# Performance work log

Hardware: AMD Instinct MI355X
Metric: run time of the kernel (lower is better)

The kernel has to match this reference:

```python
import jax, jax.numpy as jnp
import numpy as np

H = 256
T = 2048
B = 64


def setup_inputs() -> dict:
    key = jax.random.key(0)
    ks = jax.random.split(key, 10)
    s = 1.0 / np.sqrt(H)
    return {
        "x": jax.random.normal(ks[0], (T, B, H), dtype=jnp.float32),
        # AttentionLayer params
        "W_b": jax.random.normal(ks[1], (H, H), dtype=jnp.float32) * s,
        "b_b": jnp.zeros((H,), dtype=jnp.float32),
        "v_b": jax.random.normal(ks[2], (1, H), dtype=jnp.float32) * s,
        "W_e": jax.random.normal(ks[3], (H, 2 * H), dtype=jnp.float32) * s,
        "b_e": jnp.zeros((H,), dtype=jnp.float32),
        # LSTMCell params (PyTorch layout: [4H, H], gate order i,f,g,o)
        "W_ih": jax.random.uniform(ks[4], (4 * H, H), dtype=jnp.float32, minval=-s, maxval=s),
        "W_hh": jax.random.uniform(ks[5], (4 * H, H), dtype=jnp.float32, minval=-s, maxval=s),
        "b_ih": jax.random.uniform(ks[6], (4 * H,), dtype=jnp.float32, minval=-s, maxval=s),
        "b_hh": jax.random.uniform(ks[7], (4 * H,), dtype=jnp.float32, minval=-s, maxval=s),
    }


def reference(x, W_b, b_b, v_b, W_e, b_e, W_ih, W_hh, b_ih, b_hh):
    # x: [T, B, H]. Effective recurrence per timestep (inner per-sample loop in
    # the original is dead code: its output writes are overwritten and its
    # states start from zeros each iteration).
    def step(carry, xi):
        h, c = carry  # [B, H] each
        hc = jnp.concatenate([h, c], axis=1)  # [B, 2H]
        a = hc @ W_e.T + b_e                  # [B, H]
        b = xi @ W_b.T + b_b                  # [B, H]
        j = jnp.tanh(a + b) @ v_b.T           # [B, 1]
        w = jax.nn.softmax(j, axis=0) * xi    # softmax over batch dim, [B, H]
        gates = w @ W_ih.T + b_ih + h @ W_hh.T + b_hh  # [B, 4H]
        i_g, f_g, g_g, o_g = jnp.split(gates, 4, axis=1)
        c_new = jax.nn.sigmoid(f_g) * c + jax.nn.sigmoid(i_g) * jnp.tanh(g_g)
        h_new = jax.nn.sigmoid(o_g) * jnp.tanh(c_new)
        return (h_new, c_new), h_new

    Bn, Hn = x.shape[1], x.shape[2]
    init = (jnp.zeros((Bn, Hn), x.dtype), jnp.zeros((Bn, Hn), x.dtype))
    _, output = jax.lax.scan(step, init, x)  # [T, B, H]
    return output
```

## Files before the change

### kernel.cpp

```cpp
#include <hip/hip_runtime.h>
#include <math.h>

constexpr int H   = 256;
constexpr int B   = 64;
constexpr int T   = 2048;
constexpr int G   = 64;
constexpr int NTH = 512;
constexpr int HB  = H * B;

struct SharedMain {
    float wU[256][16];
    float wV[256][16];
    float wA[768][4];
    float U[64][17];
    float V[64][17];
    float ap[64][5];
    alignas(16) float outst[64][4];
    float jp[8][64];
    float bg[16];
    float ba[4];
    float v4[4];
    float s[64];
};
union SharedAll {
    SharedMain m;
    float tile[64][65];
};

__device__ __forceinline__ float sigmoidf_(float v) {
    return 1.0f / (1.0f + expf(-v));
}

__device__ __forceinline__ void grid_barrier(unsigned* bar, unsigned target) {
    __syncthreads();
    if (threadIdx.x == 0) {
        __threadfence();
        __hip_atomic_fetch_add(bar, 1u, __ATOMIC_ACQ_REL, __HIP_MEMORY_SCOPE_AGENT);
        while (__hip_atomic_load(bar, __ATOMIC_ACQUIRE, __HIP_MEMORY_SCOPE_AGENT) < target) {
            __builtin_amdgcn_s_sleep(1);
        }
        __threadfence();
    }
    __syncthreads();
}

__global__ void __launch_bounds__(NTH, 1)
scan_kernel(const float* __restrict__ x,
            const float* __restrict__ W_b,  const float* __restrict__ b_b,
            const float* __restrict__ v_b,  const float* __restrict__ W_e,
            const float* __restrict__ b_e,  const float* __restrict__ W_ih,
            const float* __restrict__ W_hh, const float* __restrict__ b_ih,
            const float* __restrict__ b_hh,
            float* __restrict__ out, float* __restrict__ wsf,
            unsigned* __restrict__ bar)
{
    __shared__ SharedAll sh;
    const int tid = threadIdx.x;
    const int g   = blockIdx.x;

    float* pJ = wsf + 64;
    float* hT = pJ + G * 64;
    float* cT = hT + HB;
    float* xT = out;

    for (int tl = g; tl < T * 4; tl += G) {
        const int t  = tl >> 2;
        const int kc = (tl & 3) << 6;
        __syncthreads();
        for (int q = tid; q < 1024; q += NTH) {
            const int r  = q >> 4;
            const int c4 = (q & 15) << 2;
            const float4 v = *(const float4*)(x + (size_t)t * HB + (size_t)r * H + kc + c4);
            sh.tile[r][c4 + 0] = v.x; sh.tile[r][c4 + 1] = v.y;
            sh.tile[r][c4 + 2] = v.z; sh.tile[r][c4 + 3] = v.w;
        }
        __syncthreads();
        for (int q = tid; q < 1024; q += NTH) {
            const int k  = q >> 4;
            const int b4 = (q & 15) << 2;
            float4 v;
            v.x = sh.tile[b4 + 0][k]; v.y = sh.tile[b4 + 1][k];
            v.z = sh.tile[b4 + 2][k]; v.w = sh.tile[b4 + 3][k];
            *(float4*)(xT + (size_t)t * HB + (size_t)(kc + k) * B + b4) = v;
        }
    }
    __syncthreads();

    for (int e = tid; e < 256 * 16; e += NTH) {
        const int k  = e >> 4;
        const int cl = e & 15;
        const int gate = cl >> 2, oi = cl & 3;
        const int row = gate * H + 4 * g + oi;
        sh.m.wU[k][cl] = W_ih[(size_t)row * H + k];
        sh.m.wV[k][cl] = W_hh[(size_t)row * H + k];
    }
    for (int e = tid; e < 768 * 4; e += NTH) {
        const int r = e >> 2;
        const int i = e & 3;
        const int col = 4 * g + i;
        float w;
        if (r < 512) w = W_e[(size_t)col * 512 + r];
        else         w = W_b[(size_t)col * 256 + (r - 512)];
        sh.m.wA[r][i] = w;
    }
    if (tid < 16) {
        const int gate = tid >> 2, oi = tid & 3;
        const int col = gate * H + 4 * g + oi;
        sh.m.bg[tid] = b_ih[col] + b_hh[col];
    }
    if (tid < 4) {
        sh.m.ba[tid] = b_e[4 * g + tid] + b_b[4 * g + tid];
        sh.m.v4[tid] = v_b[4 * g + tid];
    }
    hT[g * NTH + tid] = 0.0f;

    unsigned nb = 0;
    ++nb; grid_barrier(bar, nb * (unsigned)G);

    const int wv = tid >> 6;
    const int b  = tid & 63;

    for (int t = 0; t < T; ++t) {
        for (int e = tid; e < 64 * 17; e += NTH) { (&sh.m.U[0][0])[e] = 0.0f; (&sh.m.V[0][0])[e] = 0.0f; }
        for (int e = tid; e < 64 * 5; e += NTH) (&sh.m.ap[0][0])[e] = 0.0f;
        __syncthreads();

        if (wv < 4) {
            const int krow = wv << 6;
            const float* src = xT + (size_t)t * HB + (size_t)krow * B;
            float aU[16], aA[4];
            #pragma unroll
            for (int c = 0; c < 16; ++c) aU[c] = 0.0f;
            aA[0] = aA[1] = aA[2] = aA[3] = 0.0f;
            #pragma unroll 4
            for (int kk = 0; kk < 64; ++kk) {
                const float xv = src[kk * B + b];
                const float* wr = sh.m.wU[krow + kk];
                #pragma unroll
                for (int c = 0; c < 16; ++c) aU[c] = fmaf(xv, wr[c], aU[c]);
                const float* wa = sh.m.wA[512 + krow + kk];
                #pragma unroll
                for (int i = 0; i < 4; ++i) aA[i] = fmaf(xv, wa[i], aA[i]);
            }
            #pragma unroll
            for (int c = 0; c < 16; ++c) atomicAdd(&sh.m.U[b][c], aU[c]);
            #pragma unroll
            for (int i = 0; i < 4; ++i) atomicAdd(&sh.m.ap[b][i], aA[i]);
        } else {
            const int krow = (wv - 4) << 6;
            const float* sH = hT + (size_t)krow * B;
            const float* sC = cT + (size_t)krow * B;
            float aV[16], aA[4];
            #pragma unroll
            for (int c = 0; c < 16; ++c) aV[c] = 0.0f;
            aA[0] = aA[1] = aA[2] = aA[3] = 0.0f;
            #pragma unroll 4
            for (int kk = 0; kk < 64; ++kk) {
                const float hv = sH[kk * B + b];
                const float cv = sC[kk * B + b];
                const float* wr = sh.m.wV[krow + kk];
                #pragma unroll
                for (int c = 0; c < 16; ++c) aV[c] = fmaf(hv, wr[c], aV[c]);
                const float* waH = sh.m.wA[krow + kk];
                const float* waC = sh.m.wA[256 + krow + kk];
                #pragma unroll
                for (int i = 0; i < 4; ++i) aA[i] = fmaf(hv, waH[i], fmaf(cv, waC[i], aA[i]));
            }
            #pragma unroll
            for (int c = 0; c < 16; ++c) atomicAdd(&sh.m.V[b][c], aV[c]);
            #pragma unroll
            for (int i = 0; i < 4; ++i) atomicAdd(&sh.m.ap[b][i], aA[i]);
        }
        __syncthreads();

        if (tid < 64) {
            float pj = 0.0f;
            #pragma unroll
            for (int i = 0; i < 4; ++i)
                pj += tanhf(sh.m.ap[tid][i] + sh.m.ba[i]) * sh.m.v4[i];
            pJ[g * 64 + tid] = pj;
        }
        ++nb; grid_barrier(bar, nb * (unsigned)G);

        {
            float jpart = 0.0f;
            const int base = wv * 8;
            #pragma unroll
            for (int gg = 0; gg < 8; ++gg) jpart += pJ[(base + gg) * 64 + b];
            sh.m.jp[wv][b] = jpart;
        }
        __syncthreads();
        if (tid < 64) {
            float jv = 0.0f;
            #pragma unroll
            for (int w = 0; w < 8; ++w) jv += sh.m.jp[w][tid];
            float mx = jv;
            #pragma unroll
            for (int off = 32; off; off >>= 1) mx = fmaxf(mx, __shfl_xor(mx, off));
            const float e = expf(jv - mx);
            float ssum = e;
            #pragma unroll
            for (int off = 32; off; off >>= 1) ssum += __shfl_xor(ssum, off);
            sh.m.s[tid] = e / ssum;
        }
        __syncthreads();

        if (tid < 256) {
            const int oi = tid >> 6;
            const int bb = tid & 63;
            const float sb = sh.m.s[bb];
            const float pI = fmaf(sb, sh.m.U[bb][0  + oi], sh.m.V[bb][0  + oi]) + sh.m.bg[0  + oi];
            const float pF = fmaf(sb, sh.m.U[bb][4  + oi], sh.m.V[bb][4  + oi]) + sh.m.bg[4  + oi];
            const float pG = fmaf(sb, sh.m.U[bb][8  + oi], sh.m.V[bb][8  + oi]) + sh.m.bg[8  + oi];
            const float pO = fmaf(sb, sh.m.U[bb][12 + oi], sh.m.V[bb][12 + oi]) + sh.m.bg[12 + oi];
            const int col = 4 * g + oi;
            const float cold = cT[col * B + bb];
            const float cnew = sigmoidf_(pF) * cold + sigmoidf_(pI) * tanhf(pG);
            const float hnew = sigmoidf_(pO) * tanhf(cnew);
            cT[col * B + bb] = cnew;
            hT[col * B + bb] = hnew;
            sh.m.outst[bb][oi] = hnew;
        }
        __syncthreads();
        if (tid < 64) {
            const float4 v = *(const float4*)sh.m.outst[tid];
            *(float4*)(out + (size_t)t * HB + (size_t)tid * H + 4 * g) = v;
        }
        ++nb; grid_barrier(bar, nb * (unsigned)G);
    }
}

extern "C" void kernel_launch(void* const* d_in, const int* in_sizes, int n_in,
                              void* d_out, int out_size, void* d_ws, size_t ws_size,
                              hipStream_t stream) {
    const float* x    = (const float*)d_in[0];
    const float* W_b  = (const float*)d_in[1];
    const float* b_b  = (const float*)d_in[2];
    const float* v_b  = (const float*)d_in[3];
    const float* W_e  = (const float*)d_in[4];
    const float* b_e  = (const float*)d_in[5];
    const float* W_ih = (const float*)d_in[6];
    const float* W_hh = (const float*)d_in[7];
    const float* b_ih = (const float*)d_in[8];
    const float* b_hh = (const float*)d_in[9];
    float*    out = (float*)d_out;
    float*    wsf = (float*)d_ws;
    unsigned* bar = (unsigned*)d_ws;

    hipMemsetAsync(d_ws, 0, 256, stream);

    void* args[] = { &x, &W_b, &b_b, &v_b, &W_e, &b_e, &W_ih, &W_hh, &b_ih, &b_hh,
                     &out, &wsf, &bar };
    hipLaunchCooperativeKernel((void*)scan_kernel, dim3(G), dim3(NTH), args, 0, stream);
}
```

Baseline: 89.88 ms.

## Overlap next-step x projection with grid barrier waits using split arrive/wait epochs

Replaces the full grid barriers with split arrive/wait epoch counters, so each block signals arrival and then computes the x-dependent projection for the next timestep (double-buffered in shared memory) while other blocks catch up. All 8 waves now share the h/c recurrent reduction instead of half doing x and half doing h. The cell state is kept in shared memory rather than re-read from global. Global h/c/pJ traffic uses relaxed agent-scope atomic loads and stores with no fences, which risks memory-ordering issues. The added shared buffers raise LDS use.

```diff
diff --git a/kernel.cpp b/kernel.cpp
--- a/kernel.cpp
+++ b/kernel.cpp
@@ -12,11 +12,13 @@
     float wU[256][16];
     float wV[256][16];
     float wA[768][4];
-    float U[64][17];
+    float U[2][64][17];
+    float aX[2][64][5];
     float V[64][17];
-    float ap[64][5];
+    float aH[64][5];
     alignas(16) float outst[64][4];
     float jp[8][64];
+    float cloc[4][64];
     float bg[16];
     float ba[4];
     float v4[4];
@@ -31,7 +33,14 @@
     return 1.0f / (1.0f + expf(-v));
 }
 
-__device__ __forceinline__ void grid_barrier(unsigned* bar, unsigned target) {
+__device__ __forceinline__ float gload(const float* p) {
+    return __hip_atomic_load(p, __ATOMIC_RELAXED, __HIP_MEMORY_SCOPE_AGENT);
+}
+__device__ __forceinline__ void gstore(float* p, float v) {
+    __hip_atomic_store(p, v, __ATOMIC_RELAXED, __HIP_MEMORY_SCOPE_AGENT);
+}
+
+__device__ __forceinline__ void grid_barrier_full(unsigned* bar, unsigned target) {
     __syncthreads();
     if (threadIdx.x == 0) {
         __threadfence();
@@ -42,6 +51,18 @@
         __threadfence();
     }
     __syncthreads();
+}
+
+__device__ __forceinline__ void epoch_wait(unsigned* bar, unsigned target) {
+    if (threadIdx.x == 0) {
+        while (__hip_atomic_load(bar, __ATOMIC_RELAXED, __HIP_MEMORY_SCOPE_AGENT) < target) {
+            __builtin_amdgcn_s_sleep(1);
+        }
+    }
+    __syncthreads();
+}
+__device__ __forceinline__ void epoch_arrive(unsigned* bar) {
+    __hip_atomic_fetch_add(bar, 1u, __ATOMIC_RELAXED, __HIP_MEMORY_SCOPE_AGENT);
 }
 
 __global__ void __launch_bounds__(NTH, 1)
@@ -57,6 +78,8 @@
     __shared__ SharedAll sh;
     const int tid = threadIdx.x;
     const int g   = blockIdx.x;
+    const int wv  = tid >> 6;
+    const int b   = tid & 63;
 
     float* pJ = wsf + 64;
     float* hT = pJ + G * 64;
@@ -114,50 +137,59 @@
     }
     hT[g * NTH + tid] = 0.0f;
 
-    unsigned nb = 0;
-    ++nb; grid_barrier(bar, nb * (unsigned)G);
-
-    const int wv = tid >> 6;
-    const int b  = tid & 63;
+    grid_barrier_full(bar, (unsigned)G);
+
+    auto x_zero = [&](int p) {
+        for (int e = tid; e < 64 * 17; e += NTH) (&sh.m.U[p][0][0])[e] = 0.0f;
+        for (int e = tid; e < 64 * 5;  e += NTH) (&sh.m.aX[p][0][0])[e] = 0.0f;
+    };
+    auto x_accum = [&](int t, int p, int half) {
+        const int krow = (wv << 4) + (half << 7);
+        const float* src = xT + (size_t)t * HB + (size_t)krow * B;
+        float aU[16], aA[4];
+        #pragma unroll
+        for (int c = 0; c < 16; ++c) aU[c] = 0.0f;
+        aA[0] = aA[1] = aA[2] = aA[3] = 0.0f;
+        #pragma unroll 4
+        for (int kk = 0; kk < 16; ++kk) {
+            const float xv = src[kk * B + b];
+            const float* wr = sh.m.wU[krow + kk];
+            #pragma unroll
+            for (int c = 0; c < 16; ++c) aU[c] = fmaf(xv, wr[c], aU[c]);
+            const float* wa = sh.m.wA[512 + krow + kk];
+            #pragma unroll
+            for (int i = 0; i < 4; ++i) aA[i] = fmaf(xv, wa[i], aA[i]);
+        }
+        #pragma unroll
+        for (int c = 0; c < 16; ++c) atomicAdd(&sh.m.U[p][b][c], aU[c]);
+        #pragma unroll
+        for (int i = 0; i < 4; ++i) atomicAdd(&sh.m.aX[p][b][i], aA[i]);
+    };
+
+    int par = 0;
+    if (tid < 256) sh.m.cloc[tid >> 6][tid & 63] = 0.0f;
+    for (int e = tid; e < 64 * 17; e += NTH) (&sh.m.V[0][0])[e] = 0.0f;
+    for (int e = tid; e < 64 * 5;  e += NTH) (&sh.m.aH[0][0])[e] = 0.0f;
+    x_zero(0);
+    __syncthreads();
+    x_accum(0, 0, 0);
+    x_accum(0, 0, 1);
 
     for (int t = 0; t < T; ++t) {
-        for (int e = tid; e < 64 * 17; e += NTH) { (&sh.m.U[0][0])[e] = 0.0f; (&sh.m.V[0][0])[e] = 0.0f; }
-        for (int e = tid; e < 64 * 5; e += NTH) (&sh.m.ap[0][0])[e] = 0.0f;
-        __syncthreads();
-
-        if (wv < 4) {
-            const int krow = wv << 6;
-            const float* src = xT + (size_t)t * HB + (size_t)krow * B;
-            float aU[16], aA[4];
-            #pragma unroll
-            for (int c = 0; c < 16; ++c) aU[c] = 0.0f;
-            aA[0] = aA[1] = aA[2] = aA[3] = 0.0f;
-            #pragma unroll 4
-            for (int kk = 0; kk < 64; ++kk) {
-                const float xv = src[kk * B + b];
-                const float* wr = sh.m.wU[krow + kk];
-                #pragma unroll
-                for (int c = 0; c < 16; ++c) aU[c] = fmaf(xv, wr[c], aU[c]);
-                const float* wa = sh.m.wA[512 + krow + kk];
-                #pragma unroll
-                for (int i = 0; i < 4; ++i) aA[i] = fmaf(xv, wa[i], aA[i]);
-            }
-            #pragma unroll
-            for (int c = 0; c < 16; ++c) atomicAdd(&sh.m.U[b][c], aU[c]);
-            #pragma unroll
-            for (int i = 0; i < 4; ++i) atomicAdd(&sh.m.ap[b][i], aA[i]);
-        } else {
-            const int krow = (wv - 4) << 6;
-            const float* sH = hT + (size_t)krow * B;
-            const float* sC = cT + (size_t)krow * B;
+        if (t > 0) epoch_wait(bar, (unsigned)(2 * t + 1) * G);
+
+        {
+            const int krow = wv << 5;
+            const float* sHp = hT + (size_t)krow * B;
+            const float* sCp = cT + (size_t)krow * B;
             float aV[16], aA[4];
             #pragma unroll
             for (int c = 0; c < 16; ++c) aV[c] = 0.0f;
             aA[0] = aA[1] = aA[2] = aA[3] = 0.0f;
-            #pragma unroll 4
-            for (int kk = 0; kk < 64; ++kk) {
-                const float hv = sH[kk * B + b];
-                const float cv = sC[kk * B + b];
+            #pragma unroll 8
+            for (int kk = 0; kk < 32; ++kk) {
+                const float hv = gload(sHp + kk * B + b);
+                const float cv = gload(sCp + kk * B + b);
                 const float* wr = sh.m.wV[krow + kk];
                 #pragma unroll
                 for (int c = 0; c < 16; ++c) aV[c] = fmaf(hv, wr[c], aV[c]);
@@ -169,7 +201,7 @@
             #pragma unroll
             for (int c = 0; c < 16; ++c) atomicAdd(&sh.m.V[b][c], aV[c]);
             #pragma unroll
-            for (int i = 0; i < 4; ++i) atomicAdd(&sh.m.ap[b][i], aA[i]);
+            for (int i = 0; i < 4; ++i) atomicAdd(&sh.m.aH[b][i], aA[i]);
         }
         __syncthreads();
 
@@ -177,16 +209,21 @@
             float pj = 0.0f;
             #pragma unroll
             for (int i = 0; i < 4; ++i)
-                pj += tanhf(sh.m.ap[tid][i] + sh.m.ba[i]) * sh.m.v4[i];
-            pJ[g * 64 + tid] = pj;
-        }
-        ++nb; grid_barrier(bar, nb * (unsigned)G);
+                pj += tanhf(sh.m.aX[par][tid][i] + sh.m.aH[tid][i] + sh.m.ba[i]) * sh.m.v4[i];
+            gstore(&pJ[g * 64 + tid], pj);
+        }
+        __syncthreads();
+        if (tid == 0) epoch_arrive(bar);
+
+        if (t + 1 < T) { x_zero(par ^ 1); __syncthreads(); x_accum(t + 1, par ^ 1, 0); }
+
+        epoch_wait(bar, (unsigned)(2 * t + 2) * G);
 
         {
             float jpart = 0.0f;
             const int base = wv * 8;
             #pragma unroll
-            for (int gg = 0; gg < 8; ++gg) jpart += pJ[(base + gg) * 64 + b];
+            for (int gg = 0; gg < 8; ++gg) jpart += gload(&pJ[(base + gg) * 64 + b]);
             sh.m.jp[wv][b] = jpart;
         }
         __syncthreads();
@@ -209,24 +246,34 @@
             const int oi = tid >> 6;
             const int bb = tid & 63;
             const float sb = sh.m.s[bb];
-            const float pI = fmaf(sb, sh.m.U[bb][0  + oi], sh.m.V[bb][0  + oi]) + sh.m.bg[0  + oi];
-            const float pF = fmaf(sb, sh.m.U[bb][4  + oi], sh.m.V[bb][4  + oi]) + sh.m.bg[4  + oi];
-            const float pG = fmaf(sb, sh.m.U[bb][8  + oi], sh.m.V[bb][8  + oi]) + sh.m.bg[8  + oi];
-            const float pO = fmaf(sb, sh.m.U[bb][12 + oi], sh.m.V[bb][12 + oi]) + sh.m.bg[12 + oi];
+            const float* Ur = sh.m.U[par][bb];
+            const float* Vr = sh.m.V[bb];
+            const float pI = fmaf(sb, Ur[0  + oi], Vr[0  + oi]) + sh.m.bg[0  + oi];
+            const float pF = fmaf(sb, Ur[4  + oi], Vr[4  + oi]) + sh.m.bg[4  + oi];
+            const float pG = fmaf(sb, Ur[8  + oi], Vr[8  + oi]) + sh.m.bg[8  + oi];
+            const float pO = fmaf(sb, Ur[12 + oi], Vr[12 + oi]) + sh.m.bg[12 + oi];
             const int col = 4 * g + oi;
-            const float cold = cT[col * B + bb];
+            const float cold = sh.m.cloc[oi][bb];
             const float cnew = sigmoidf_(pF) * cold + sigmoidf_(pI) * tanhf(pG);
             const float hnew = sigmoidf_(pO) * tanhf(cnew);
-            cT[col * B + bb] = cnew;
-            hT[col * B + bb] = hnew;
+            sh.m.cloc[oi][bb] = cnew;
+            gstore(&cT[(size_t)col * B + bb], cnew);
+            gstore(&hT[(size_t)col * B + bb], hnew);
             sh.m.outst[bb][oi] = hnew;
         }
         __syncthreads();
+
         if (tid < 64) {
             const float4 v = *(const float4*)sh.m.outst[tid];
             *(float4*)(out + (size_t)t * HB + (size_t)tid * H + 4 * g) = v;
         }
-        ++nb; grid_barrier(bar, nb * (unsigned)G);
+        for (int e = tid; e < 64 * 17; e += NTH) (&sh.m.V[0][0])[e] = 0.0f;
+        for (int e = tid; e < 64 * 5;  e += NTH) (&sh.m.aH[0][0])[e] = 0.0f;
+        __syncthreads();
+        if (tid == 0) epoch_arrive(bar);
+
+        if (t + 1 < T) x_accum(t + 1, par ^ 1, 1);
+        par ^= 1;
     }
 }
 
```

After: 118.9 ms. 1.32x slower.

## Partition recurrence by batch sample per block with flag-based softmax exchange

Applied to the files above, without the earlier changes.

Each block now owns one batch sample and keeps its full h and c in shared memory. The old split across hidden columns needed two grid barriers per step and global h/c traffic; the only cross-block exchange left is the per-sample attention score, published through versioned 64-bit slots that a single wave polls. Weights are streamed from global memory/L2 every step instead of being held in LDS, and the next step's x·W_b projection is computed ahead of time. The x transpose prologue is also removed.

```diff
diff --git a/kernel.cpp b/kernel.cpp
--- a/kernel.cpp
+++ b/kernel.cpp
@@ -5,43 +5,32 @@
 constexpr int B   = 64;
 constexpr int T   = 2048;
 constexpr int G   = 64;
-constexpr int NTH = 512;
+constexpr int NTH = 1024;
 constexpr int HB  = H * B;
 
-struct SharedMain {
-    float wU[256][16];
-    float wV[256][16];
-    float wA[768][4];
-    float U[64][17];
-    float V[64][17];
-    float ap[64][5];
-    alignas(16) float outst[64][4];
-    float jp[8][64];
-    float bg[16];
-    float ba[4];
-    float v4[4];
-    float s[64];
+struct Sh {
+    float h[H];
+    float c[H];
+    float xv[2][H];
+    float bx[2][H];
+    float a_s[H];
+    float Ux[4*H];
+    float Vh[4*H];
+    float bg[4*H];
+    float ba[H];
+    float vb[H];
+    float jp[4];
+    float sb;
 };
-union SharedAll {
-    SharedMain m;
-    float tile[64][65];
-};
-
-__device__ __forceinline__ float sigmoidf_(float v) {
-    return 1.0f / (1.0f + expf(-v));
-}
-
-__device__ __forceinline__ void grid_barrier(unsigned* bar, unsigned target) {
-    __syncthreads();
-    if (threadIdx.x == 0) {
-        __threadfence();
-        __hip_atomic_fetch_add(bar, 1u, __ATOMIC_ACQ_REL, __HIP_MEMORY_SCOPE_AGENT);
-        while (__hip_atomic_load(bar, __ATOMIC_ACQUIRE, __HIP_MEMORY_SCOPE_AGENT) < target) {
-            __builtin_amdgcn_s_sleep(1);
-        }
-        __threadfence();
-    }
-    __syncthreads();
+
+__device__ __forceinline__ float sigmoidf_(float v) { return 1.0f / (1.0f + expf(-v)); }
+
+__device__ __forceinline__ float dot4(float4 w, float4 m, float acc) {
+    acc = fmaf(w.x, m.x, acc);
+    acc = fmaf(w.y, m.y, acc);
+    acc = fmaf(w.z, m.z, acc);
+    acc = fmaf(w.w, m.w, acc);
+    return acc;
 }
 
 __global__ void __launch_bounds__(NTH, 1)
@@ -51,182 +40,159 @@
             const float* __restrict__ b_e,  const float* __restrict__ W_ih,
             const float* __restrict__ W_hh, const float* __restrict__ b_ih,
             const float* __restrict__ b_hh,
-            float* __restrict__ out, float* __restrict__ wsf,
-            unsigned* __restrict__ bar)
+            float* __restrict__ out,
+            unsigned long long* __restrict__ slot)
 {
-    __shared__ SharedAll sh;
-    const int tid = threadIdx.x;
-    const int g   = blockIdx.x;
-
-    float* pJ = wsf + 64;
-    float* hT = pJ + G * 64;
-    float* cT = hT + HB;
-    float* xT = out;
-
-    for (int tl = g; tl < T * 4; tl += G) {
-        const int t  = tl >> 2;
-        const int kc = (tl & 3) << 6;
-        __syncthreads();
-        for (int q = tid; q < 1024; q += NTH) {
-            const int r  = q >> 4;
-            const int c4 = (q & 15) << 2;
-            const float4 v = *(const float4*)(x + (size_t)t * HB + (size_t)r * H + kc + c4);
-            sh.tile[r][c4 + 0] = v.x; sh.tile[r][c4 + 1] = v.y;
-            sh.tile[r][c4 + 2] = v.z; sh.tile[r][c4 + 3] = v.w;
-        }
-        __syncthreads();
-        for (int q = tid; q < 1024; q += NTH) {
-            const int k  = q >> 4;
-            const int b4 = (q & 15) << 2;
-            float4 v;
-            v.x = sh.tile[b4 + 0][k]; v.y = sh.tile[b4 + 1][k];
-            v.z = sh.tile[b4 + 2][k]; v.w = sh.tile[b4 + 3][k];
-            *(float4*)(xT + (size_t)t * HB + (size_t)(kc + k) * B + b4) = v;
-        }
+    __shared__ Sh sh;
+    const int tid  = threadIdx.x;
+    const int g    = blockIdx.x;
+    const int wv   = tid >> 6;
+    const int lane = tid & 63;
+    const int oct  = lane >> 3;
+    const int q    = lane & 7;
+
+    sh.bg[tid] = b_ih[tid] + b_hh[tid];
+    if (tid < H) {
+        sh.h[tid] = 0.0f; sh.c[tid] = 0.0f;
+        sh.ba[tid] = b_e[tid] + b_b[tid];
+        sh.vb[tid] = v_b[tid];
+    }
+    if (tid < 64) {
+        float4 v = *(const float4*)(x + (size_t)g * H + (size_t)tid * 4);
+        *(float4*)&sh.xv[0][tid * 4] = v;
     }
     __syncthreads();
-
-    for (int e = tid; e < 256 * 16; e += NTH) {
-        const int k  = e >> 4;
-        const int cl = e & 15;
-        const int gate = cl >> 2, oi = cl & 3;
-        const int row = gate * H + 4 * g + oi;
-        sh.m.wU[k][cl] = W_ih[(size_t)row * H + k];
-        sh.m.wV[k][cl] = W_hh[(size_t)row * H + k];
-    }
-    for (int e = tid; e < 768 * 4; e += NTH) {
-        const int r = e >> 2;
-        const int i = e & 3;
-        const int col = 4 * g + i;
-        float w;
-        if (r < 512) w = W_e[(size_t)col * 512 + r];
-        else         w = W_b[(size_t)col * 256 + (r - 512)];
-        sh.m.wA[r][i] = w;
-    }
-    if (tid < 16) {
-        const int gate = tid >> 2, oi = tid & 3;
-        const int col = gate * H + 4 * g + oi;
-        sh.m.bg[tid] = b_ih[col] + b_hh[col];
-    }
-    if (tid < 4) {
-        sh.m.ba[tid] = b_e[4 * g + tid] + b_b[4 * g + tid];
-        sh.m.v4[tid] = v_b[4 * g + tid];
-    }
-    hT[g * NTH + tid] = 0.0f;
-
-    unsigned nb = 0;
-    ++nb; grid_barrier(bar, nb * (unsigned)G);
-
-    const int wv = tid >> 6;
-    const int b  = tid & 63;
-
+    {
+        const float4* xv4 = (const float4*)sh.xv[0];
+        #pragma unroll
+        for (int p = 0; p < 2; ++p) {
+            const int r = wv * 16 + p * 8 + oct;
+            const float4* wr4 = (const float4*)(W_b + (size_t)r * H);
+            float acc = 0.0f;
+            #pragma unroll
+            for (int j = 0; j < 8; ++j)
+                acc = dot4(wr4[j * 8 + q], xv4[j * 8 + q], acc);
+            acc += __shfl_xor(acc, 1); acc += __shfl_xor(acc, 2); acc += __shfl_xor(acc, 4);
+            if (q == 0) sh.bx[0][r] = acc;
+        }
+    }
+    __syncthreads();
+
+    int par = 0;
     for (int t = 0; t < T; ++t) {
-        for (int e = tid; e < 64 * 17; e += NTH) { (&sh.m.U[0][0])[e] = 0.0f; (&sh.m.V[0][0])[e] = 0.0f; }
-        for (int e = tid; e < 64 * 5; e += NTH) (&sh.m.ap[0][0])[e] = 0.0f;
-        __syncthreads();
-
-        if (wv < 4) {
-            const int krow = wv << 6;
-            const float* src = xT + (size_t)t * HB + (size_t)krow * B;
-            float aU[16], aA[4];
-            #pragma unroll
-            for (int c = 0; c < 16; ++c) aU[c] = 0.0f;
-            aA[0] = aA[1] = aA[2] = aA[3] = 0.0f;
-            #pragma unroll 4
-            for (int kk = 0; kk < 64; ++kk) {
-                const float xv = src[kk * B + b];
-                const float* wr = sh.m.wU[krow + kk];
-                #pragma unroll
-                for (int c = 0; c < 16; ++c) aU[c] = fmaf(xv, wr[c], aU[c]);
-                const float* wa = sh.m.wA[512 + krow + kk];
-                #pragma unroll
-                for (int i = 0; i < 4; ++i) aA[i] = fmaf(xv, wa[i], aA[i]);
-            }
-            #pragma unroll
-            for (int c = 0; c < 16; ++c) atomicAdd(&sh.m.U[b][c], aU[c]);
-            #pragma unroll
-            for (int i = 0; i < 4; ++i) atomicAdd(&sh.m.ap[b][i], aA[i]);
-        } else {
-            const int krow = (wv - 4) << 6;
-            const float* sH = hT + (size_t)krow * B;
-            const float* sC = cT + (size_t)krow * B;
-            float aV[16], aA[4];
-            #pragma unroll
-            for (int c = 0; c < 16; ++c) aV[c] = 0.0f;
-            aA[0] = aA[1] = aA[2] = aA[3] = 0.0f;
-            #pragma unroll 4
-            for (int kk = 0; kk < 64; ++kk) {
-                const float hv = sH[kk * B + b];
-                const float cv = sC[kk * B + b];
-                const float* wr = sh.m.wV[krow + kk];
-                #pragma unroll
-                for (int c = 0; c < 16; ++c) aV[c] = fmaf(hv, wr[c], aV[c]);
-                const float* waH = sh.m.wA[krow + kk];
-                const float* waC = sh.m.wA[256 + krow + kk];
-                #pragma unroll
-                for (int i = 0; i < 4; ++i) aA[i] = fmaf(hv, waH[i], fmaf(cv, waC[i], aA[i]));
-            }
-            #pragma unroll
-            for (int c = 0; c < 16; ++c) atomicAdd(&sh.m.V[b][c], aV[c]);
-            #pragma unroll
-            for (int i = 0; i < 4; ++i) atomicAdd(&sh.m.ap[b][i], aA[i]);
-        }
-        __syncthreads();
-
+        {
+            const float4* hv4 = (const float4*)sh.h;
+            const float4* cv4 = (const float4*)sh.c;
+            #pragma unroll
+            for (int p = 0; p < 2; ++p) {
+                const int r = wv * 16 + p * 8 + oct;
+                const float4* wr4 = (const float4*)(W_e + (size_t)r * (2 * H));
+                float acc = 0.0f;
+                #pragma unroll
+                for (int j = 0; j < 8; ++j)
+                    acc = dot4(wr4[j * 8 + q], hv4[j * 8 + q], acc);
+                #pragma unroll
+                for (int j = 0; j < 8; ++j)
+                    acc = dot4(wr4[64 + j * 8 + q], cv4[j * 8 + q], acc);
+                acc += __shfl_xor(acc, 1); acc += __shfl_xor(acc, 2); acc += __shfl_xor(acc, 4);
+                if (q == 0) sh.a_s[r] = acc;
+            }
+        }
+        __syncthreads();
+        if (tid < H) {
+            float tv = tanhf(sh.a_s[tid] + sh.bx[par][tid] + sh.ba[tid]) * sh.vb[tid];
+            #pragma unroll
+            for (int off = 32; off; off >>= 1) tv += __shfl_xor(tv, off);
+            if (lane == 0) sh.jp[wv] = tv;
+        }
+        __syncthreads();
+        if (tid == 0) {
+            float jv = sh.jp[0] + sh.jp[1] + sh.jp[2] + sh.jp[3];
+            unsigned long long u = ((unsigned long long)(unsigned)(t + 1) << 32)
+                                 | (unsigned long long)__float_as_uint(jv);
+            __hip_atomic_store(&slot[(size_t)(t & 1) * G + g], u,
+                               __ATOMIC_RELAXED, __HIP_MEMORY_SCOPE_AGENT);
+        }
+
+        const int parn = par ^ 1;
+        const int tn = (t + 1 < T) ? (t + 1) : t;
         if (tid < 64) {
-            float pj = 0.0f;
-            #pragma unroll
-            for (int i = 0; i < 4; ++i)
-                pj += tanhf(sh.m.ap[tid][i] + sh.m.ba[i]) * sh.m.v4[i];
-            pJ[g * 64 + tid] = pj;
-        }
-        ++nb; grid_barrier(bar, nb * (unsigned)G);
-
+            float4 v = *(const float4*)(x + ((size_t)tn * B + g) * H + (size_t)tid * 4);
+            *(float4*)&sh.xv[parn][tid * 4] = v;
+        }
         {
-            float jpart = 0.0f;
-            const int base = wv * 8;
-            #pragma unroll
-            for (int gg = 0; gg < 8; ++gg) jpart += pJ[(base + gg) * 64 + b];
-            sh.m.jp[wv][b] = jpart;
-        }
-        __syncthreads();
-        if (tid < 64) {
-            float jv = 0.0f;
-            #pragma unroll
-            for (int w = 0; w < 8; ++w) jv += sh.m.jp[w][tid];
+            const float4* xv4 = (const float4*)sh.xv[par];
+            const float4* hv4 = (const float4*)sh.h;
+            #pragma unroll 2
+            for (int p = 0; p < 8; ++p) {
+                const int r = wv * 64 + p * 8 + oct;
+                const float4* wi4 = (const float4*)(W_ih + (size_t)r * H);
+                const float4* wh4 = (const float4*)(W_hh + (size_t)r * H);
+                float aU = 0.0f, aV = 0.0f;
+                #pragma unroll
+                for (int j = 0; j < 8; ++j) {
+                    const float4 xm = xv4[j * 8 + q];
+                    const float4 hm = hv4[j * 8 + q];
+                    aU = dot4(wi4[j * 8 + q], xm, aU);
+                    aV = dot4(wh4[j * 8 + q], hm, aV);
+                }
+                aU += __shfl_xor(aU, 1); aU += __shfl_xor(aU, 2); aU += __shfl_xor(aU, 4);
+                aV += __shfl_xor(aV, 1); aV += __shfl_xor(aV, 2); aV += __shfl_xor(aV, 4);
+                if (q == 0) { sh.Ux[r] = aU; sh.Vh[r] = aV; }
+            }
+        }
+        __syncthreads();
+        {
+            const float4* xv4 = (const float4*)sh.xv[parn];
+            #pragma unroll
+            for (int p = 0; p < 2; ++p) {
+                const int r = wv * 16 + p * 8 + oct;
+                const float4* wr4 = (const float4*)(W_b + (size_t)r * H);
+                float acc = 0.0f;
+                #pragma unroll
+                for (int j = 0; j < 8; ++j)
+                    acc = dot4(wr4[j * 8 + q], xv4[j * 8 + q], acc);
+                acc += __shfl_xor(acc, 1); acc += __shfl_xor(acc, 2); acc += __shfl_xor(acc, 4);
+                if (q == 0) sh.bx[parn][r] = acc;
+            }
+        }
+
+        if (wv == 0) {
+            const unsigned want = (unsigned)(t + 1);
+            unsigned long long u;
+            for (;;) {
+                u = __hip_atomic_load(&slot[(size_t)(t & 1) * G + lane],
+                                      __ATOMIC_RELAXED, __HIP_MEMORY_SCOPE_AGENT);
+                if (__all((int)((unsigned)(u >> 32) == want))) break;
+                __builtin_amdgcn_s_sleep(1);
+            }
+            float jv = __uint_as_float((unsigned)u);
             float mx = jv;
             #pragma unroll
             for (int off = 32; off; off >>= 1) mx = fmaxf(mx, __shfl_xor(mx, off));
-            const float e = expf(jv - mx);
-            float ssum = e;
-            #pragma unroll
-            for (int off = 32; off; off >>= 1) ssum += __shfl_xor(ssum, off);
-            sh.m.s[tid] = e / ssum;
-        }
-        __syncthreads();
-
-        if (tid < 256) {
-            const int oi = tid >> 6;
-            const int bb = tid & 63;
-            const float sb = sh.m.s[bb];
-            const float pI = fmaf(sb, sh.m.U[bb][0  + oi], sh.m.V[bb][0  + oi]) + sh.m.bg[0  + oi];
-            const float pF = fmaf(sb, sh.m.U[bb][4  + oi], sh.m.V[bb][4  + oi]) + sh.m.bg[4  + oi];
-            const float pG = fmaf(sb, sh.m.U[bb][8  + oi], sh.m.V[bb][8  + oi]) + sh.m.bg[8  + oi];
-            const float pO = fmaf(sb, sh.m.U[bb][12 + oi], sh.m.V[bb][12 + oi]) + sh.m.bg[12 + oi];
-            const int col = 4 * g + oi;
-            const float cold = cT[col * B + bb];
-            const float cnew = sigmoidf_(pF) * cold + sigmoidf_(pI) * tanhf(pG);
-            const float hnew = sigmoidf_(pO) * tanhf(cnew);
-            cT[col * B + bb] = cnew;
-            hT[col * B + bb] = hnew;
-            sh.m.outst[bb][oi] = hnew;
-        }
-        __syncthreads();
-        if (tid < 64) {
-            const float4 v = *(const float4*)sh.m.outst[tid];
-            *(float4*)(out + (size_t)t * HB + (size_t)tid * H + 4 * g) = v;
-        }
-        ++nb; grid_barrier(bar, nb * (unsigned)G);
+            float e = expf(jv - mx);
+            float ss = e;
+            #pragma unroll
+            for (int off = 32; off; off >>= 1) ss += __shfl_xor(ss, off);
+            float sv = __shfl(e, g) / ss;
+            if (lane == 0) sh.sb = sv;
+        }
+        __syncthreads();
+
+        if (tid < H) {
+            const float sbv = sh.sb;
+            const int n = tid;
+            const float gi = fmaf(sbv, sh.Ux[n        ], sh.Vh[n        ]) + sh.bg[n        ];
+            const float gf = fmaf(sbv, sh.Ux[n +     H], sh.Vh[n +     H]) + sh.bg[n +     H];
+            const float gG = fmaf(sbv, sh.Ux[n + 2 * H], sh.Vh[n + 2 * H]) + sh.bg[n + 2 * H];
+            const float go = fmaf(sbv, sh.Ux[n + 3 * H], sh.Vh[n + 3 * H]) + sh.bg[n + 3 * H];
+            const float cnew = sigmoidf_(gf) * sh.c[n] + sigmoidf_(gi) * tanhf(gG);
+            const float hnew = sigmoidf_(go) * tanhf(cnew);
+            sh.c[n] = cnew; sh.h[n] = hnew;
+            out[(size_t)t * HB + (size_t)g * H + n] = hnew;
+        }
+        __syncthreads();
+        par = parn;
     }
 }
 
@@ -243,13 +209,12 @@
     const float* W_hh = (const float*)d_in[7];
     const float* b_ih = (const float*)d_in[8];
     const float* b_hh = (const float*)d_in[9];
-    float*    out = (float*)d_out;
-    float*    wsf = (float*)d_ws;
-    unsigned* bar = (unsigned*)d_ws;
-
-    hipMemsetAsync(d_ws, 0, 256, stream);
+    float* out = (float*)d_out;
+    unsigned long long* slot = (unsigned long long*)d_ws;
+
+    hipMemsetAsync(d_ws, 0, 1024, stream);
 
     void* args[] = { &x, &W_b, &b_b, &v_b, &W_e, &b_e, &W_ih, &W_hh, &b_ih, &b_hh,
-                     &out, &wsf, &bar };
+                     &out, &slot };
     hipLaunchCooperativeKernel((void*)scan_kernel, dim3(G), dim3(NTH), args, 0, stream);
 }
```

Measured after the change: 114.8 ms. 1.28x slower.
